# Performance work log

Measured on AMD Instinct MI355X. Metric: run time of the kernel, lower is better.

## Reference

```python
import jax, jax.numpy as jnp
import numpy as np

K = 4  # neighbors per node (init kwarg)


def setup_inputs() -> dict:
    key = jax.random.key(0)
    node_features = jax.random.normal(key, (8, 4096, 256), dtype=jnp.float32)
    return {"node_features": node_features}


def reference(node_features):
    # node_features: (B, N, C)
    B, N, C = node_features.shape
    k = min(K, N - 1)
    # cosine metric: L2-normalize rows, then pairwise dot products
    fn = node_features / jnp.linalg.norm(node_features, axis=-1, keepdims=True)
    sim = jnp.einsum("bnc,bmc->bnm", fn, fn)  # (B, N, N)
    # exclude self-loops: fill diagonal with -inf
    diag = jnp.eye(N, dtype=bool)
    sim = jnp.where(diag[None, :, :], -jnp.inf, sim)
    topk_values, topk_indices = jax.lax.top_k(sim, k)  # (B, N, k)
    # edge list per batch: source i repeated k times, target = topk index
    src = jnp.broadcast_to(jnp.arange(N)[:, None], (N, k)).reshape(-1)  # (N*k,)
    src = jnp.broadcast_to(src[None, :], (B, N * k))
    tgt = topk_indices.reshape(B, N * k)
    edge_index = jnp.stack([src, tgt], axis=1)  # (B, 2, N*k)
    edge_weight = topk_values.reshape(B, N * k)  # (B, N*k)
    return edge_index, edge_weight
```

## Files before the change

### kernel.cpp

```cpp
#include <hip/hip_runtime.h>
#include <hip/hip_bf16.h>
#include <float.h>
#include <limits.h>

#define BATCH 8
#define NN    4096
#define CC    256
#define KNN_K 4
#define NKE   (NN * KNN_K)

#define MTI  64
#define NJ   64
#define NC8  8
#define NM6  6
#define BROW 264

typedef __attribute__((ext_vector_type(8))) short  bf16x8;
typedef __attribute__((ext_vector_type(4))) float  f32x4;

__device__ __forceinline__ short f2bf(float f) {
    unsigned u = __float_as_uint(f);
    return (short)((u + 0x7FFFu + ((u >> 16) & 1u)) >> 16);
}

__device__ __forceinline__ unsigned umin32(unsigned a, unsigned b) { return a < b ? a : b; }
__device__ __forceinline__ unsigned umax32(unsigned a, unsigned b) { return a > b ? a : b; }

__device__ __forceinline__ void pk_ins8(unsigned k, unsigned (&t)[NC8]) {
    #pragma unroll
    for (int s = NC8 - 1; s > 0; --s) t[s] = umax32(t[s], umin32(t[s - 1], k));
    t[0] = umax32(t[0], k);
}
__device__ __forceinline__ void pk_ins6(unsigned k, unsigned (&t)[NM6]) {
    #pragma unroll
    for (int s = NM6 - 1; s > 0; --s) t[s] = umax32(t[s], umin32(t[s - 1], k));
    t[0] = umax32(t[0], k);
}

__device__ __forceinline__ bool knn_better(float v, int j, float v2, int j2) {
    return (v > v2) || (v == v2 && j < j2);
}
__device__ __forceinline__ void knn_insert4(float v, int j, float (&tv)[4], int (&tj)[4]) {
    if (knn_better(v, j, tv[3], tj[3])) {
        tv[3] = v; tj[3] = j;
        #pragma unroll
        for (int s = 3; s > 0; --s) {
            if (knn_better(tv[s], tj[s], tv[s - 1], tj[s - 1])) {
                float fv = tv[s]; tv[s] = tv[s - 1]; tv[s - 1] = fv;
                int   fj = tj[s]; tj[s] = tj[s - 1]; tj[s - 1] = fj;
            }
        }
    }
}

__global__ void knn_prep_kernel(const float* __restrict__ x, float* __restrict__ invn,
                                ushort* __restrict__ xn, int write_bf16) {
    const int row  = blockIdx.x * 4 + (threadIdx.x >> 6);
    const int lane = threadIdx.x & 63;
    const float4 v = *(const float4*)(x + (size_t)row * CC + lane * 4);
    float ss = v.x * v.x + v.y * v.y + v.z * v.z + v.w * v.w;
    #pragma unroll
    for (int off = 32; off > 0; off >>= 1) ss += __shfl_down(ss, off, 64);
    const float inv = 1.0f / sqrtf(__shfl(ss, 0, 64));
    if (lane == 0) invn[row] = inv;
    if (write_bf16) {
        short4 s4;
        s4.x = f2bf(v.x * inv); s4.y = f2bf(v.y * inv);
        s4.z = f2bf(v.z * inv); s4.w = f2bf(v.w * inv);
        *(short4*)(xn + (size_t)row * CC + lane * 4) = s4;
    }
}

template<bool FROM_BF16>
__global__ __launch_bounds__(256, 3) void knn_main_kernel(
        const float* __restrict__ x, const float* __restrict__ invn,
        const ushort* __restrict__ xn, float* __restrict__ out,
        float* __restrict__ sval, int* __restrict__ sjid, int nh2) {
    __shared__ __align__(16) ushort Bsh[NJ * BROW];

    const int tid = threadIdx.x;
    const int b   = blockIdx.x & 7;
    const int t   = blockIdx.x >> 3;
    const int it   = nh2 ? (t >> 1) : t;
    const int half = nh2 ? (t & 1)  : 0;
    const int i0   = it * MTI;
    const int jbase = half * (NN / 2);
    const int nch   = nh2 ? (NN / NJ / 2) : (NN / NJ);

    const float*  xb   = x    + (size_t)b * NN * CC;
    const ushort* xnb  = xn   + (size_t)b * NN * CC;
    const float*  invb = invn + (size_t)b * NN;

    const int w  = tid >> 6;
    const int l  = tid & 63;
    const int lm = l & 15;
    const int q  = l >> 4;

    bf16x8 afrag[8];
    const int gi = i0 + w * 16 + lm;
    if (FROM_BF16) {
        #pragma unroll
        for (int kt = 0; kt < 8; ++kt)
            afrag[kt] = *(const bf16x8*)(xnb + (size_t)gi * CC + kt * 32 + q * 8);
    } else {
        const float vi = invb[gi];
        #pragma unroll
        for (int kt = 0; kt < 8; ++kt) {
            const float* src = xb + (size_t)gi * CC + kt * 32 + q * 8;
            const float4 f0 = *(const float4*)(src);
            const float4 f1 = *(const float4*)(src + 4);
            bf16x8 a;
            a[0] = f2bf(f0.x * vi); a[1] = f2bf(f0.y * vi);
            a[2] = f2bf(f0.z * vi); a[3] = f2bf(f0.w * vi);
            a[4] = f2bf(f1.x * vi); a[5] = f2bf(f1.y * vi);
            a[6] = f2bf(f1.z * vi); a[7] = f2bf(f1.w * vi);
            afrag[kt] = a;
        }
    }

    unsigned cl[4][NC8];
    #pragma unroll
    for (int r = 0; r < 4; ++r)
        #pragma unroll
        for (int s = 0; s < NC8; ++s) cl[r][s] = 0u;

    const int s_gc = tid & 31;
    const int s_r0 = tid >> 5;
    bf16x8 pregs[8];
    if (FROM_BF16) {
        #pragma unroll
        for (int lp = 0; lp < 8; ++lp)
            pregs[lp] = *(const bf16x8*)(xnb + (size_t)(jbase + s_r0 + 8 * lp) * CC + s_gc * 8);
    }

    for (int jt = 0; jt < nch; ++jt) {
        const int j0 = jbase + jt * NJ;
        __syncthreads();
        if (FROM_BF16) {
            #pragma unroll
            for (int lp = 0; lp < 8; ++lp)
                *(bf16x8*)(Bsh + (s_r0 + 8 * lp) * BROW + s_gc * 8) = pregs[lp];
        } else {
            #pragma unroll
            for (int lp = 0; lp < 16; ++lp) {
                const int u2 = tid + 256 * lp;
                const int row = u2 >> 6, c4 = u2 & 63;
                const float sc = invb[j0 + row];
                const float4 v = *(const float4*)(xb + (size_t)(j0 + row) * CC + c4 * 4);
                short4 s4;
                s4.x = f2bf(v.x * sc); s4.y = f2bf(v.y * sc);
                s4.z = f2bf(v.z * sc); s4.w = f2bf(v.w * sc);
                *(short4*)(Bsh + row * BROW + c4 * 4) = s4;
            }
        }
        __syncthreads();
        if (FROM_BF16 && jt + 1 < nch) {
            const int jn = jbase + (jt + 1) * NJ;
            #pragma unroll
            for (int lp = 0; lp < 8; ++lp)
                pregs[lp] = *(const bf16x8*)(xnb + (size_t)(jn + s_r0 + 8 * lp) * CC + s_gc * 8);
        }

        f32x4 acc[4];
        #pragma unroll
        for (int ct = 0; ct < 4; ++ct) acc[ct] = (f32x4){0.f, 0.f, 0.f, 0.f};
        #pragma unroll
        for (int kt = 0; kt < 8; ++kt) {
            #pragma unroll
            for (int ct = 0; ct < 4; ++ct) {
                const bf16x8 bf = *(const bf16x8*)(Bsh + (ct * 16 + lm) * BROW + kt * 32 + q * 8);
                acc[ct] = __builtin_amdgcn_mfma_f32_16x16x32_bf16(afrag[kt], bf, acc[ct], 0, 0, 0);
            }
        }

        const bool dchunk = (j0 == i0);
        #pragma unroll
        for (int ct = 0; ct < 4; ++ct) {
            const int jg  = j0 + ct * 16 + lm;
            const unsigned ivj = (unsigned)(4095 - jg);
            #pragma unroll
            for (int r = 0; r < 4; ++r) {
                unsigned pk = (__float_as_uint(acc[ct][r] + 2.0f) & 0xFFFFF000u) | ivj;
                if (dchunk && (w * 16 + q * 4 + r) == (ct * 16 + lm)) pk = 0u;
                pk_ins8(pk, cl[r]);
            }
        }
    }

    unsigned tm[4][NM6];
    #pragma unroll
    for (int r = 0; r < 4; ++r)
        #pragma unroll
        for (int s = 0; s < NM6; ++s) tm[r][s] = cl[r][s];
    #pragma unroll
    for (int m = 1; m <= 8; m <<= 1) {
        #pragma unroll
        for (int r = 0; r < 4; ++r) {
            unsigned pin[NM6];
            #pragma unroll
            for (int s = 0; s < NM6; ++s)
                pin[s] = (unsigned)__shfl_xor((int)tm[r][s], m, 64);
            #pragma unroll
            for (int s = 0; s < NM6; ++s) pk_ins6(pin[s], tm[r]);
        }
    }

    unsigned* cpk = (unsigned*)Bsh;
    __syncthreads();
    if (lm == 0) {
        #pragma unroll
        for (int r = 0; r < 4; ++r) {
            const int rt = w * 16 + q * 4 + r;
            #pragma unroll
            for (int s = 0; s < NM6; ++s) cpk[rt * NM6 + s] = tm[r][s];
        }
    }
    __syncthreads();

    const int rr   = tid & 63;
    const int slot = tid >> 6;
    const int ig   = i0 + rr;
    const float inv_i = invb[ig];
    const float* xi = xb + (size_t)ig * CC;
    const int ncand = (slot < 2) ? 2 : 1;
    const int cbase = (slot < 2) ? slot * 2 : 2 + slot;
    float rv[2]; int rj[2];
    for (int u = 0; u < ncand; ++u) {
        const int c  = cbase + u;
        const int jc = 4095 - (int)(cpk[rr * NM6 + c] & 0xFFFu);
        const float* xj = xb + (size_t)jc * CC;
        float d = 0.f;
        #pragma unroll 16
        for (int k4 = 0; k4 < 64; ++k4) {
            const float4 av = *(const float4*)(xi + k4 * 4);
            const float4 bv = *(const float4*)(xj + k4 * 4);
            d = fmaf(av.x, bv.x, d);
            d = fmaf(av.y, bv.y, d);
            d = fmaf(av.z, bv.z, d);
            d = fmaf(av.w, bv.w, d);
        }
        rv[u] = d * inv_i * invb[jc];
        rj[u] = jc;
    }

    if (nh2) {
        for (int u = 0; u < ncand; ++u) {
            const size_t o = ((size_t)(b * NN + ig) * 2 + half) * NM6 + (cbase + u);
            sval[o] = rv[u];
            sjid[o] = rj[u];
        }
        return;
    }

    float* cvl = (float*)(Bsh + 4096);
    for (int u = 0; u < ncand; ++u) cvl[rr * NM6 + (cbase + u)] = rv[u];
    __syncthreads();
    if (tid < MTI) {
        const int r = tid, ig2 = i0 + r;
        float fv[4]; int fj[4];
        #pragma unroll
        for (int s = 0; s < 4; ++s) { fv[s] = -INFINITY; fj[s] = INT_MAX; }
        for (int c = 0; c < NM6; ++c) {
            const int jc = 4095 - (int)(cpk[r * NM6 + c] & 0xFFFu);
            knn_insert4(cvl[r * NM6 + c], jc, fv, fj);
        }
        float* o_src = out + (size_t)b * 2 * NKE;
        float* o_tgt = o_src + NKE;
        float* o_w   = out + (size_t)BATCH * 2 * NKE + (size_t)b * NKE;
        #pragma unroll
        for (int s = 0; s < 4; ++s) {
            o_src[ig2 * KNN_K + s] = (float)ig2;
            o_tgt[ig2 * KNN_K + s] = (float)fj[s];
            o_w[ig2 * KNN_K + s]   = fv[s];
        }
    }
}

__global__ __launch_bounds__(256) void knn_select_kernel(
        const float* __restrict__ sval, const int* __restrict__ sjid,
        float* __restrict__ out) {
    const int row_g = blockIdx.x * 256 + threadIdx.x;
    const int bb = row_g >> 12, ig = row_g & (NN - 1);
    float fv[4]; int fj[4];
    #pragma unroll
    for (int s = 0; s < 4; ++s) { fv[s] = -INFINITY; fj[s] = INT_MAX; }
    const size_t base = (size_t)row_g * 2 * NM6;
    for (int c = 0; c < 2 * NM6; ++c)
        knn_insert4(sval[base + c], sjid[base + c], fv, fj);
    float* o_src = out + (size_t)bb * 2 * NKE;
    float* o_tgt = o_src + NKE;
    float* o_w   = out + (size_t)BATCH * 2 * NKE + (size_t)bb * NKE;
    #pragma unroll
    for (int s = 0; s < 4; ++s) {
        o_src[ig * KNN_K + s] = (float)ig;
        o_tgt[ig * KNN_K + s] = (float)fj[s];
        o_w[ig * KNN_K + s]   = fv[s];
    }
}

extern "C" void kernel_launch(void* const* d_in, const int* in_sizes, int n_in,
                              void* d_out, int out_size, void* d_ws, size_t ws_size,
                              hipStream_t stream) {
    const float* x    = (const float*)d_in[0];
    float*       out  = (float*)d_out;
    float*       invn = (float*)d_ws;
    ushort*      xn   = (ushort*)((char*)d_ws + 131072);
    char*        p2   = (char*)d_ws + 131072 + (size_t)BATCH * NN * CC * sizeof(ushort);
    float*       sval = (float*)p2;
    int*         sjid = (int*)(p2 + (size_t)BATCH * NN * 2 * NM6 * sizeof(float));
    const size_t need_xn  = 131072 + (size_t)BATCH * NN * CC * sizeof(ushort);
    const size_t need_all = need_xn + (size_t)BATCH * NN * 2 * NM6 * 8;

    if (ws_size >= need_all) {
        knn_prep_kernel<<<(BATCH * NN) / 4, 256, 0, stream>>>(x, invn, xn, 1);
        knn_main_kernel<true><<<BATCH * MTI * 2, 256, 0, stream>>>(x, invn, xn, out, sval, sjid, 1);
        knn_select_kernel<<<(BATCH * NN) / 256, 256, 0, stream>>>(sval, sjid, out);
    } else if (ws_size >= need_xn) {
        knn_prep_kernel<<<(BATCH * NN) / 4, 256, 0, stream>>>(x, invn, xn, 1);
        knn_main_kernel<true><<<BATCH * MTI, 256, 0, stream>>>(x, invn, xn, out, nullptr, nullptr, 0);
    } else {
        knn_prep_kernel<<<(BATCH * NN) / 4, 256, 0, stream>>>(x, invn, xn, 0);
        knn_main_kernel<false><<<BATCH * MTI, 256, 0, stream>>>(x, invn, xn, out, nullptr, nullptr, 0);
    }
}
```

Before: 257.6 us.

## Retile waves 2x2 over rows/columns and keep per-column-half top-6 candidate lists

Changes the wave decomposition so each wave computes two 16-row M tiles against one 16-column slice of a 32-wide j chunk, instead of one M tile against four column tiles. Each lane now keeps eight shorter top-6 lists rather than four top-8 lists, and the two column-halves' lists are merged later as 12 candidates per row, rescored in fp32 and selected. This is meant to cut the per-element insertion cost and the B-fragment LDS reads per MFMA. In exchange it adds more fp32 rescoring work, more barriers from halving the chunk size, and a larger scratch buffer.

```diff
diff --git a/kernel.cpp b/kernel.cpp
--- a/kernel.cpp
+++ b/kernel.cpp
@@ -10,9 +10,9 @@
 #define NKE   (NN * KNN_K)
 
 #define MTI  64
-#define NJ   64
-#define NC8  8
+#define NJ   32
 #define NM6  6
+#define NCND 12
 #define BROW 264
 
 typedef __attribute__((ext_vector_type(8))) short  bf16x8;
@@ -26,11 +26,6 @@
 __device__ __forceinline__ unsigned umin32(unsigned a, unsigned b) { return a < b ? a : b; }
 __device__ __forceinline__ unsigned umax32(unsigned a, unsigned b) { return a > b ? a : b; }
 
-__device__ __forceinline__ void pk_ins8(unsigned k, unsigned (&t)[NC8]) {
-    #pragma unroll
-    for (int s = NC8 - 1; s > 0; --s) t[s] = umax32(t[s], umin32(t[s - 1], k));
-    t[0] = umax32(t[0], k);
-}
 __device__ __forceinline__ void pk_ins6(unsigned k, unsigned (&t)[NM6]) {
     #pragma unroll
     for (int s = NM6 - 1; s > 0; --s) t[s] = umax32(t[s], umin32(t[s - 1], k));
@@ -92,44 +87,49 @@
     const float*  invb = invn + (size_t)b * NN;
 
     const int w  = tid >> 6;
+    const int wr = w & 1;
+    const int wc = w >> 1;
     const int l  = tid & 63;
     const int lm = l & 15;
     const int q  = l >> 4;
 
-    bf16x8 afrag[8];
-    const int gi = i0 + w * 16 + lm;
-    if (FROM_BF16) {
-        #pragma unroll
-        for (int kt = 0; kt < 8; ++kt)
-            afrag[kt] = *(const bf16x8*)(xnb + (size_t)gi * CC + kt * 32 + q * 8);
-    } else {
-        const float vi = invb[gi];
-        #pragma unroll
-        for (int kt = 0; kt < 8; ++kt) {
-            const float* src = xb + (size_t)gi * CC + kt * 32 + q * 8;
-            const float4 f0 = *(const float4*)(src);
-            const float4 f1 = *(const float4*)(src + 4);
-            bf16x8 a;
-            a[0] = f2bf(f0.x * vi); a[1] = f2bf(f0.y * vi);
-            a[2] = f2bf(f0.z * vi); a[3] = f2bf(f0.w * vi);
-            a[4] = f2bf(f1.x * vi); a[5] = f2bf(f1.y * vi);
-            a[6] = f2bf(f1.z * vi); a[7] = f2bf(f1.w * vi);
-            afrag[kt] = a;
-        }
-    }
-
-    unsigned cl[4][NC8];
-    #pragma unroll
-    for (int r = 0; r < 4; ++r)
-        #pragma unroll
-        for (int s = 0; s < NC8; ++s) cl[r][s] = 0u;
+    bf16x8 afrag[2][8];
+    #pragma unroll
+    for (int mi = 0; mi < 2; ++mi) {
+        const int gi = i0 + wr * 32 + mi * 16 + lm;
+        if (FROM_BF16) {
+            #pragma unroll
+            for (int kt = 0; kt < 8; ++kt)
+                afrag[mi][kt] = *(const bf16x8*)(xnb + (size_t)gi * CC + kt * 32 + q * 8);
+        } else {
+            const float vi = invb[gi];
+            #pragma unroll
+            for (int kt = 0; kt < 8; ++kt) {
+                const float* src = xb + (size_t)gi * CC + kt * 32 + q * 8;
+                const float4 f0 = *(const float4*)(src);
+                const float4 f1 = *(const float4*)(src + 4);
+                bf16x8 a;
+                a[0] = f2bf(f0.x * vi); a[1] = f2bf(f0.y * vi);
+                a[2] = f2bf(f0.z * vi); a[3] = f2bf(f0.w * vi);
+                a[4] = f2bf(f1.x * vi); a[5] = f2bf(f1.y * vi);
+                a[6] = f2bf(f1.z * vi); a[7] = f2bf(f1.w * vi);
+                afrag[mi][kt] = a;
+            }
+        }
+    }
+
+    unsigned cl[8][NM6];
+    #pragma unroll
+    for (int r = 0; r < 8; ++r)
+        #pragma unroll
+        for (int s = 0; s < NM6; ++s) cl[r][s] = 0u;
 
     const int s_gc = tid & 31;
     const int s_r0 = tid >> 5;
-    bf16x8 pregs[8];
+    bf16x8 pregs[4];
     if (FROM_BF16) {
         #pragma unroll
-        for (int lp = 0; lp < 8; ++lp)
+        for (int lp = 0; lp < 4; ++lp)
             pregs[lp] = *(const bf16x8*)(xnb + (size_t)(jbase + s_r0 + 8 * lp) * CC + s_gc * 8);
     }
 
@@ -138,11 +138,11 @@
         __syncthreads();
         if (FROM_BF16) {
             #pragma unroll
-            for (int lp = 0; lp < 8; ++lp)
+            for (int lp = 0; lp < 4; ++lp)
                 *(bf16x8*)(Bsh + (s_r0 + 8 * lp) * BROW + s_gc * 8) = pregs[lp];
         } else {
             #pragma unroll
-            for (int lp = 0; lp < 16; ++lp) {
+            for (int lp = 0; lp < 8; ++lp) {
                 const int u2 = tid + 256 * lp;
                 const int row = u2 >> 6, c4 = u2 & 63;
                 const float sc = invb[j0 + row];
@@ -157,51 +157,44 @@
         if (FROM_BF16 && jt + 1 < nch) {
             const int jn = jbase + (jt + 1) * NJ;
             #pragma unroll
-            for (int lp = 0; lp < 8; ++lp)
+            for (int lp = 0; lp < 4; ++lp)
                 pregs[lp] = *(const bf16x8*)(xnb + (size_t)(jn + s_r0 + 8 * lp) * CC + s_gc * 8);
         }
 
-        f32x4 acc[4];
-        #pragma unroll
-        for (int ct = 0; ct < 4; ++ct) acc[ct] = (f32x4){0.f, 0.f, 0.f, 0.f};
+        f32x4 acc[2];
+        acc[0] = (f32x4){0.f, 0.f, 0.f, 0.f};
+        acc[1] = (f32x4){0.f, 0.f, 0.f, 0.f};
         #pragma unroll
         for (int kt = 0; kt < 8; ++kt) {
-            #pragma unroll
-            for (int ct = 0; ct < 4; ++ct) {
-                const bf16x8 bf = *(const bf16x8*)(Bsh + (ct * 16 + lm) * BROW + kt * 32 + q * 8);
-                acc[ct] = __builtin_amdgcn_mfma_f32_16x16x32_bf16(afrag[kt], bf, acc[ct], 0, 0, 0);
-            }
-        }
-
-        const bool dchunk = (j0 == i0);
-        #pragma unroll
-        for (int ct = 0; ct < 4; ++ct) {
-            const int jg  = j0 + ct * 16 + lm;
-            const unsigned ivj = (unsigned)(4095 - jg);
+            const bf16x8 bf = *(const bf16x8*)(Bsh + (wc * 16 + lm) * BROW + kt * 32 + q * 8);
+            acc[0] = __builtin_amdgcn_mfma_f32_16x16x32_bf16(afrag[0][kt], bf, acc[0], 0, 0, 0);
+            acc[1] = __builtin_amdgcn_mfma_f32_16x16x32_bf16(afrag[1][kt], bf, acc[1], 0, 0, 0);
+        }
+
+        const bool dch = (j0 == i0 + wr * 32);
+        const int  cj  = wc * 16 + lm;
+        const unsigned ivj = (unsigned)(4095 - (j0 + cj));
+        #pragma unroll
+        for (int mi = 0; mi < 2; ++mi) {
             #pragma unroll
             for (int r = 0; r < 4; ++r) {
-                unsigned pk = (__float_as_uint(acc[ct][r] + 2.0f) & 0xFFFFF000u) | ivj;
-                if (dchunk && (w * 16 + q * 4 + r) == (ct * 16 + lm)) pk = 0u;
-                pk_ins8(pk, cl[r]);
-            }
-        }
-    }
-
-    unsigned tm[4][NM6];
-    #pragma unroll
-    for (int r = 0; r < 4; ++r)
-        #pragma unroll
-        for (int s = 0; s < NM6; ++s) tm[r][s] = cl[r][s];
+                unsigned pk = (__float_as_uint(acc[mi][r] + 2.0f) & 0xFFFFF000u) | ivj;
+                if (dch && cj == (mi * 16 + q * 4 + r)) pk = 0u;
+                pk_ins6(pk, cl[mi * 4 + r]);
+            }
+        }
+    }
+
     #pragma unroll
     for (int m = 1; m <= 8; m <<= 1) {
         #pragma unroll
-        for (int r = 0; r < 4; ++r) {
+        for (int r = 0; r < 8; ++r) {
             unsigned pin[NM6];
             #pragma unroll
             for (int s = 0; s < NM6; ++s)
-                pin[s] = (unsigned)__shfl_xor((int)tm[r][s], m, 64);
-            #pragma unroll
-            for (int s = 0; s < NM6; ++s) pk_ins6(pin[s], tm[r]);
+                pin[s] = (unsigned)__shfl_xor((int)cl[r][s], m, 64);
+            #pragma unroll
+            for (int s = 0; s < NM6; ++s) pk_ins6(pin[s], cl[r]);
         }
     }
 
@@ -209,11 +202,14 @@
     __syncthreads();
     if (lm == 0) {
         #pragma unroll
-        for (int r = 0; r < 4; ++r) {
-            const int rt = w * 16 + q * 4 + r;
-            #pragma unroll
-            for (int s = 0; s < NM6; ++s) cpk[rt * NM6 + s] = tm[r][s];
-        }
+        for (int mi = 0; mi < 2; ++mi)
+            #pragma unroll
+            for (int r = 0; r < 4; ++r) {
+                const int rt = wr * 32 + mi * 16 + q * 4 + r;
+                #pragma unroll
+                for (int s = 0; s < NM6; ++s)
+                    cpk[(rt * 2 + wc) * NM6 + s] = cl[mi * 4 + r][s];
+            }
     }
     __syncthreads();
 
@@ -222,12 +218,11 @@
     const int ig   = i0 + rr;
     const float inv_i = invb[ig];
     const float* xi = xb + (size_t)ig * CC;
-    const int ncand = (slot < 2) ? 2 : 1;
-    const int cbase = (slot < 2) ? slot * 2 : 2 + slot;
-    float rv[2]; int rj[2];
-    for (int u = 0; u < ncand; ++u) {
-        const int c  = cbase + u;
-        const int jc = 4095 - (int)(cpk[rr * NM6 + c] & 0xFFFu);
+    float rv[3]; int rj[3];
+    #pragma unroll
+    for (int u = 0; u < 3; ++u) {
+        const int c  = slot * 3 + u;
+        const int jc = 4095 - (int)(cpk[rr * NCND + c] & 0xFFFu);
         const float* xj = xb + (size_t)jc * CC;
         float d = 0.f;
         #pragma unroll 16
@@ -244,8 +239,9 @@
     }
 
     if (nh2) {
-        for (int u = 0; u < ncand; ++u) {
-            const size_t o = ((size_t)(b * NN + ig) * 2 + half) * NM6 + (cbase + u);
+        #pragma unroll
+        for (int u = 0; u < 3; ++u) {
+            const size_t o = ((size_t)(b * NN + ig) * 2 + half) * NCND + (slot * 3 + u);
             sval[o] = rv[u];
             sjid[o] = rj[u];
         }
@@ -253,16 +249,17 @@
     }
 
     float* cvl = (float*)(Bsh + 4096);
-    for (int u = 0; u < ncand; ++u) cvl[rr * NM6 + (cbase + u)] = rv[u];
+    #pragma unroll
+    for (int u = 0; u < 3; ++u) cvl[rr * NCND + (slot * 3 + u)] = rv[u];
     __syncthreads();
     if (tid < MTI) {
         const int r = tid, ig2 = i0 + r;
         float fv[4]; int fj[4];
         #pragma unroll
         for (int s = 0; s < 4; ++s) { fv[s] = -INFINITY; fj[s] = INT_MAX; }
-        for (int c = 0; c < NM6; ++c) {
-            const int jc = 4095 - (int)(cpk[r * NM6 + c] & 0xFFFu);
-            knn_insert4(cvl[r * NM6 + c], jc, fv, fj);
+        for (int c = 0; c < NCND; ++c) {
+            const int jc = 4095 - (int)(cpk[r * NCND + c] & 0xFFFu);
+            knn_insert4(cvl[r * NCND + c], jc, fv, fj);
         }
         float* o_src = out + (size_t)b * 2 * NKE;
         float* o_tgt = o_src + NKE;
@@ -284,8 +281,8 @@
     float fv[4]; int fj[4];
     #pragma unroll
     for (int s = 0; s < 4; ++s) { fv[s] = -INFINITY; fj[s] = INT_MAX; }
-    const size_t base = (size_t)row_g * 2 * NM6;
-    for (int c = 0; c < 2 * NM6; ++c)
+    const size_t base = (size_t)row_g * 2 * NCND;
+    for (int c = 0; c < 2 * NCND; ++c)
         knn_insert4(sval[base + c], sjid[base + c], fv, fj);
     float* o_src = out + (size_t)bb * 2 * NKE;
     float* o_tgt = o_src + NKE;
@@ -307,19 +304,19 @@
     ushort*      xn   = (ushort*)((char*)d_ws + 131072);
     char*        p2   = (char*)d_ws + 131072 + (size_t)BATCH * NN * CC * sizeof(ushort);
     float*       sval = (float*)p2;
-    int*         sjid = (int*)(p2 + (size_t)BATCH * NN * 2 * NM6 * sizeof(float));
+    int*         sjid = (int*)(p2 + (size_t)BATCH * NN * 2 * NCND * sizeof(float));
     const size_t need_xn  = 131072 + (size_t)BATCH * NN * CC * sizeof(ushort);
-    const size_t need_all = need_xn + (size_t)BATCH * NN * 2 * NM6 * 8;
+    const size_t need_all = need_xn + (size_t)BATCH * NN * 2 * NCND * 8;
 
     if (ws_size >= need_all) {
         knn_prep_kernel<<<(BATCH * NN) / 4, 256, 0, stream>>>(x, invn, xn, 1);
-        knn_main_kernel<true><<<BATCH * MTI * 2, 256, 0, stream>>>(x, invn, xn, out, sval, sjid, 1);
+        knn_main_kernel<true><<<BATCH * (NN / MTI) * 2, 256, 0, stream>>>(x, invn, xn, out, sval, sjid, 1);
         knn_select_kernel<<<(BATCH * NN) / 256, 256, 0, stream>>>(sval, sjid, out);
     } else if (ws_size >= need_xn) {
         knn_prep_kernel<<<(BATCH * NN) / 4, 256, 0, stream>>>(x, invn, xn, 1);
-        knn_main_kernel<true><<<BATCH * MTI, 256, 0, stream>>>(x, invn, xn, out, nullptr, nullptr, 0);
+        knn_main_kernel<true><<<BATCH * (NN / MTI), 256, 0, stream>>>(x, invn, xn, out, nullptr, nullptr, 0);
     } else {
         knn_prep_kernel<<<(BATCH * NN) / 4, 256, 0, stream>>>(x, invn, xn, 0);
-        knn_main_kernel<false><<<BATCH * MTI, 256, 0, stream>>>(x, invn, xn, out, nullptr, nullptr, 0);
-    }
-}
+        knn_main_kernel<false><<<BATCH * (NN / MTI), 256, 0, stream>>>(x, invn, xn, out, nullptr, nullptr, 0);
+    }
+}
```

After: 382.6 us. +48.5%, slower.
